# Performance work log

Measured on AMD Instinct MI355X. Metric: run time of the kernel, lower is better.

Reference implementation:

```python
import jax, jax.numpy as jnp
from jax import lax
import numpy as np

B, C, Hf, Wf = 4, 256, 64, 64
COMP = max(C // 4, 16)  # 64
SCALE, K_UP, K_ENC = 2, 5, 3
EPS = 1e-5


def setup_inputs() -> dict:
    key = jax.random.key(0)
    ks = jax.random.split(key, 6)
    x = jax.random.normal(ks[0], (B, C, Hf, Wf), dtype=jnp.float32)
    w_comp = jax.random.normal(ks[1], (COMP, C), dtype=jnp.float32) * (1.0 / np.sqrt(C))
    bn_gamma = jnp.ones((COMP,), dtype=jnp.float32)
    bn_beta = jnp.zeros((COMP,), dtype=jnp.float32)
    bn_mean = jax.random.normal(ks[2], (COMP,), dtype=jnp.float32) * 0.1
    bn_var = jax.random.uniform(ks[3], (COMP,), dtype=jnp.float32, minval=0.5, maxval=1.5)
    w_enc = jax.random.normal(ks[4], (K_UP * K_UP * SCALE * SCALE, COMP, K_ENC, K_ENC), dtype=jnp.float32) * (1.0 / np.sqrt(COMP * K_ENC * K_ENC))
    return {"x": x, "w_comp": w_comp, "bn_gamma": bn_gamma, "bn_beta": bn_beta,
            "bn_mean": bn_mean, "bn_var": bn_var, "w_enc": w_enc}


def reference(x, w_comp, bn_gamma, bn_beta, bn_mean, bn_var, w_enc):
    b, c, h, w = x.shape
    s, k = SCALE, K_UP
    # 1x1 compression conv
    comp = jnp.einsum('bchw,oc->bohw', x, w_comp)
    # BatchNorm (eval-style, running stats) + SiLU
    inv = (bn_gamma / jnp.sqrt(bn_var + EPS))[:, None, None]
    bn = (comp - bn_mean[:, None, None]) * inv + bn_beta[:, None, None]
    act = bn * jax.nn.sigmoid(bn)
    # encoder conv -> per-pixel reassembly kernels, channels = k^2 * s^2 (k2 outer, s2 inner)
    mask = lax.conv_general_dilated(act, w_enc, (1, 1), ((1, 1), (1, 1)),
                                    dimension_numbers=('NCHW', 'OIHW', 'NCHW'))
    mask = mask.reshape(b, k * k, s * s, h, w)
    mask = jax.nn.softmax(mask, axis=1)  # softmax over k_up*k_up window
    # unfold: gather 5x5 neighborhoods (pad 2), k = dy*5+dx row-major like F.unfold
    pad = k // 2
    xp = jnp.pad(x, ((0, 0), (0, 0), (pad, pad), (pad, pad)))
    patches = jnp.stack([xp[:, :, dy:dy + h, dx:dx + w]
                         for dy in range(k) for dx in range(k)], axis=2)  # (b,c,k2,h,w)
    # content-aware weighted sum per sub-pixel position
    out = jnp.einsum('bksij,bckij->bcsij', mask, patches)  # (b,c,s2,h,w)
    # s2 -> (s0,s1); pixel (i*s+s0, j*s+s1)
    out = out.reshape(b, c, s, s, h, w).transpose(0, 1, 4, 2, 5, 3).reshape(b, c, h * s, w * s)
    return out
```

## Files before the change

### kernel.cpp

```cpp
#include <hip/hip_runtime.h>
#include <hip/hip_bf16.h>
#include <hip/hip_fp16.h>
#include <math.h>

#define B_ 4
#define C_ 256
#define H_ 64
#define W_ 64
#define COMP_ 64
#define K2_ 25
#define HW_ (H_*W_)
#define EPS_ 1e-5f
#define WTE_STRIDE 26

typedef float v2f __attribute__((ext_vector_type(2)));
#define FMA2(a, b, c) __builtin_elementwise_fma((a), (b), (c))

__global__ void k_transpose(const float* __restrict__ w_comp,
                            const float* __restrict__ w_enc,
                            float* __restrict__ wTc,
                            float* __restrict__ wTe) {
    int t = blockIdx.x * 256 + threadIdx.x;
    if (t < COMP_ * C_) {
        int o = t & 63;
        int c = t >> 6;
        wTc[t] = w_comp[o * C_ + c];
    } else {
        int t2 = t - COMP_ * C_;
        if (t2 < 100 * COMP_ * 9) {
            int k2 = t2 % 25;
            int r = t2 / 25;
            int s2 = r & 3; r >>= 2;
            int q = r % 9;
            int o = r / 9;
            wTe[((o * 9 + q) * 4 + s2) * WTE_STRIDE + k2] =
                w_enc[(((k2 * 4 + s2) * COMP_) + o) * 9 + q];
        }
    }
}

__global__ void __launch_bounds__(512)
k_compress(const float* __restrict__ x, const float* __restrict__ wTc,
           const float* __restrict__ gamma, const float* __restrict__ beta,
           const float* __restrict__ mean, const float* __restrict__ var,
           float* __restrict__ act) {
    __shared__ float sx[256 * 68];
    const int tx = threadIdx.x;
    const int ty = threadIdx.y;
    const int tid = ty * 64 + tx;
    const int ogu = __builtin_amdgcn_readfirstlane(ty);
    const int b = blockIdx.y;
    const int p0 = blockIdx.x * 64;

    const float* xb = x + (size_t)b * C_ * HW_ + p0;
#pragma unroll
    for (int l = 0; l < 8; ++l) {
        int e = tid + l * 512;
        int c = e >> 4;
        int p4 = (e & 15) << 2;
        float4 v4 = *(const float4*)(xb + (size_t)c * HW_ + p4);
        *(float4*)&sx[c * 68 + p4] = v4;
    }
    __syncthreads();

    v2f acc2[4];
#pragma unroll
    for (int k = 0; k < 4; ++k) acc2[k] = (v2f){0.f, 0.f};

#pragma unroll 8
    for (int c = 0; c < 256; ++c) {
        float xv = sx[c * 68 + tx];
        const v2f* w2 = (const v2f*)(wTc + c * COMP_ + ogu * 8);
        v2f xv2 = (v2f){xv, xv};
#pragma unroll
        for (int k = 0; k < 4; ++k)
            acc2[k] = FMA2(xv2, w2[k], acc2[k]);
    }

#pragma unroll
    for (int k = 0; k < 4; ++k) {
        int o0 = ty * 8 + 2 * k;
#pragma unroll
        for (int h = 0; h < 2; ++h) {
            int o = o0 + h;
            float sv = (h == 0) ? acc2[k].x : acc2[k].y;
            float iv = gamma[o] * rsqrtf(var[o] + EPS_);
            float bn = (sv - mean[o]) * iv + beta[o];
            float sg = 1.f / (1.f + __expf(-bn));
            act[((b * COMP_ + o) * HW_) + p0 + tx] = bn * sg;
        }
    }
}

__global__ void __launch_bounds__(1024)
k_encoder(const float* __restrict__ act, const float* __restrict__ wTe,
          __half* __restrict__ maskT) {
    __shared__ float sact[13312];
    const int tx = threadIdx.x;
    const int ty = threadIdx.y;
    const int tz = threadIdx.z;
    const int tid = (tz * 4 + ty) * 64 + tx;
    const int i = blockIdx.x;
    const int b = blockIdx.y;
    const int s2u = __builtin_amdgcn_readfirstlane(ty);
    const int ogu = __builtin_amdgcn_readfirstlane(tz);

    const float* ab = act + (size_t)b * COMP_ * HW_;
    for (int t = tid; t < 3 * COMP_ * 66; t += 1024) {
        int col = t % 66;
        int r = t / 66;
        int o = r & 63;
        int row = r >> 6;
        int gi = i + row - 1;
        int gj = col - 1;
        float v = 0.f;
        if ((unsigned)gi < 64u && (unsigned)gj < 64u)
            v = ab[(o * H_ + gi) * W_ + gj];
        sact[t] = v;
    }
    __syncthreads();

    v2f acc2[13];
#pragma unroll
    for (int k = 0; k < 13; ++k) acc2[k] = (v2f){0.f, 0.f};

#pragma unroll 2
    for (int oi = 0; oi < 16; ++oi) {
        int o = ogu * 16 + oi;
#pragma unroll
        for (int q = 0; q < 9; ++q) {
            const int dy = q / 3, dx = q % 3;
            float a = sact[(dy * COMP_ + o) * 66 + tx + dx];
            const float* wb = wTe + ((o * 9 + q) * 4 + s2u) * WTE_STRIDE;
            const v2f* w2 = (const v2f*)wb;
            v2f a2 = (v2f){a, a};
#pragma unroll
            for (int k = 0; k < 12; ++k)
                acc2[k] = FMA2(a2, w2[k], acc2[k]);
            acc2[12].x = fmaf(wb[24], a, acc2[12].x);
        }
    }
    __syncthreads();

    v2f* bufA = (v2f*)sact;
    v2f* bufB = bufA + 3328;
    const int rix = ty * 64 + tx;
    if (tz == 1) {
#pragma unroll
        for (int k = 0; k < 13; ++k) bufA[k * 256 + rix] = acc2[k];
    } else if (tz == 2) {
#pragma unroll
        for (int k = 0; k < 13; ++k) bufB[k * 256 + rix] = acc2[k];
    }
    __syncthreads();
    if (tz == 0) {
#pragma unroll
        for (int k = 0; k < 13; ++k) acc2[k] += bufA[k * 256 + rix];
    } else if (tz == 3) {
#pragma unroll
        for (int k = 0; k < 13; ++k) acc2[k] += bufB[k * 256 + rix];
    }
    __syncthreads();
    if (tz == 3) {
#pragma unroll
        for (int k = 0; k < 13; ++k) bufA[k * 256 + rix] = acc2[k];
    }
    __syncthreads();
    float ex[K2_];
    if (tz == 0) {
#pragma unroll
        for (int k = 0; k < 13; ++k) acc2[k] += bufA[k * 256 + rix];

        float mx = acc2[12].x;
#pragma unroll
        for (int k = 0; k < 12; ++k) mx = fmaxf(mx, fmaxf(acc2[k].x, acc2[k].y));
        float sum = 0.f;
#pragma unroll
        for (int k = 0; k < 12; ++k) {
            ex[2 * k]     = __expf(acc2[k].x - mx);
            ex[2 * k + 1] = __expf(acc2[k].y - mx);
            sum += ex[2 * k] + ex[2 * k + 1];
        }
        ex[24] = __expf(acc2[12].x - mx);
        sum += ex[24];
        float rs = 1.f / sum;
#pragma unroll
        for (int k = 0; k < K2_; ++k) ex[k] *= rs;
    }
    __syncthreads();

    __half* st = (__half*)sact;
    if (tz == 0) {
#pragma unroll
        for (int k = 0; k < K2_; ++k)
            st[tx * 100 + k * 4 + ty] = __float2half(ex[k]);
    }
    __syncthreads();

    float4* dst = (float4*)(maskT + ((size_t)b * HW_ + i * 64) * 100);
    const float4* src = (const float4*)st;
    if (tid < 800) dst[tid] = src[tid];
}

__global__ void __launch_bounds__(256)
k_reassemble(const float* __restrict__ x, const __half* __restrict__ maskT,
             float* __restrict__ out) {
    __shared__ __align__(16) __half smask[64 * 100];
    __shared__ __align__(16) float sx[5 * 68 * 20];
    const int tx = threadIdx.x;
    const int ty = threadIdx.y;
    const int tid = ty * 64 + tx;

    const int bid = blockIdx.x;
    const int wg  = ((bid & 7) << 9) | (bid >> 3);
    const int cc = wg & 15;
    const int i  = (wg >> 4) & 63;
    const int b  = wg >> 10;

    const float4* msrc = (const float4*)(maskT + ((size_t)b * HW_ + i * 64) * 100);
    float4 vm[4];
#pragma unroll
    for (int t = 0; t < 4; ++t) {
        int e = tid + t * 256;
        vm[t] = (e < 800) ? msrc[e] : make_float4(0.f, 0.f, 0.f, 0.f);
    }

    float4 vx[6];
#pragma unroll
    for (int l = 0; l < 6; ++l) {
        int e = tid + l * 256;
        int q = e / 340;
        int rem = e - q * 340;
        int r = rem / 68;
        int col = rem - r * 68;
        int gi = i + r - 2;
        int gj = col - 2;
        float4 v = make_float4(0.f, 0.f, 0.f, 0.f);
        if (e < 1360 && (unsigned)gi < 64u && (unsigned)gj < 64u) {
            const float* p = x + ((size_t)b * C_ + cc * 16 + q * 4) * HW_ + gi * W_ + gj;
            v.x = p[0];
            v.y = p[HW_];
            v.z = p[2 * HW_];
            v.w = p[3 * HW_];
        }
        vx[l] = v;
    }

    {
        float4* mdst = (float4*)smask;
#pragma unroll
        for (int t = 0; t < 4; ++t) {
            int e = tid + t * 256;
            if (e < 800) mdst[e] = vm[t];
        }
    }
#pragma unroll
    for (int l = 0; l < 6; ++l) {
        int e = tid + l * 256;
        if (e < 1360) {
            int q = e / 340;
            int rem = e - q * 340;
            int r = rem / 68;
            int col = rem - r * 68;
            *(float4*)&sx[(r * 68 + col) * 20 + q * 4] = vx[l];
        }
    }
    __syncthreads();

    v2f a01[4], a23[4];
#pragma unroll
    for (int cl = 0; cl < 4; ++cl) { a01[cl] = (v2f){0.f, 0.f}; a23[cl] = (v2f){0.f, 0.f}; }

    float4 xq = *(const float4*)&sx[(0 * 68 + tx + 0) * 20 + ty * 4];
    __half2 h01 = *(const __half2*)&smask[tx * 100 + 0];
    __half2 h23 = *(const __half2*)&smask[tx * 100 + 2];

#pragma unroll
    for (int k2 = 0; k2 < K2_; ++k2) {
        float4 xq_c = xq;
        __half2 h01_c = h01, h23_c = h23;
        if (k2 < K2_ - 1) {
            const int kn = k2 + 1;
            const int dy = kn / 5, dx = kn % 5;
            xq  = *(const float4*)&sx[(dy * 68 + tx + dx) * 20 + ty * 4];
            h01 = *(const __half2*)&smask[tx * 100 + kn * 4];
            h23 = *(const __half2*)&smask[tx * 100 + kn * 4 + 2];
        }
        float2 f01 = __half22float2(h01_c);
        float2 f23 = __half22float2(h23_c);
        v2f m01 = (v2f){f01.x, f01.y};
        v2f m23 = (v2f){f23.x, f23.y};
        float xc[4] = {xq_c.x, xq_c.y, xq_c.z, xq_c.w};
#pragma unroll
        for (int cl = 0; cl < 4; ++cl) {
            v2f xv2 = (v2f){xc[cl], xc[cl]};
            a01[cl] = FMA2(xv2, m01, a01[cl]);
            a23[cl] = FMA2(xv2, m23, a23[cl]);
        }
    }

#pragma unroll
    for (int cl = 0; cl < 4; ++cl) {
        int c = cc * 16 + ty * 4 + cl;
        float* op = out + (((size_t)(b * C_ + c) * 128 + 2 * i) * 128) + 2 * tx;
        *(float2*)op         = float2{a01[cl].x, a01[cl].y};
        *(float2*)(op + 128) = float2{a23[cl].x, a23[cl].y};
    }
}

extern "C" void kernel_launch(void* const* d_in, const int* in_sizes, int n_in,
                              void* d_out, int out_size, void* d_ws, size_t ws_size,
                              hipStream_t stream) {
    const float* x       = (const float*)d_in[0];
    const float* w_comp  = (const float*)d_in[1];
    const float* bn_g    = (const float*)d_in[2];
    const float* bn_b    = (const float*)d_in[3];
    const float* bn_m    = (const float*)d_in[4];
    const float* bn_v    = (const float*)d_in[5];
    const float* w_enc   = (const float*)d_in[6];
    float* out = (float*)d_out;

    float* ws    = (float*)d_ws;
    float* wTc   = ws;
    float* wTe   = ws + 16384;
    float* act   = ws + 16384 + 59904;
    __half* maskT = (__half*)(act + (size_t)B_ * COMP_ * HW_);

    k_transpose<<<289, 256, 0, stream>>>(w_comp, w_enc, wTc, wTe);
    k_compress<<<dim3(64, B_), dim3(64, 8), 0, stream>>>(x, wTc, bn_g, bn_b, bn_m, bn_v, act);
    k_encoder<<<dim3(64, B_), dim3(64, 4, 4), 0, stream>>>(act, wTe, maskT);
    k_reassemble<<<4096, dim3(64, 4), 0, stream>>>(x, maskT, out);
}
```

Measured before the change: 163.4 us.

## Double-buffer reassembly with direct global-to-LDS loads and split encoder across s2 halves

The reassembly kernel becomes persistent-style. 512 blocks each loop over 8 (batch, channel-group) tiles and use double-buffered LDS filled by global_load_lds. This is meant to overlap loading the x rows and the mask with the FMA work and to cut launch and occupancy waste. The encoder grid doubles by splitting the four sub-pixel outputs across blockIdx.z, with 512-thread blocks, which raises block count but recomputes the shared activation tile load per half. The LDS layout for x changes to channel-major rows, which adds extra zero-padding passes.

```diff
diff --git a/kernel.cpp b/kernel.cpp
--- a/kernel.cpp
+++ b/kernel.cpp
@@ -15,6 +15,15 @@
 
 typedef float v2f __attribute__((ext_vector_type(2)));
 #define FMA2(a, b, c) __builtin_elementwise_fma((a), (b), (c))
+
+__device__ __forceinline__ void gload4(const void* g, void* l) {
+    __builtin_amdgcn_global_load_lds((const __attribute__((address_space(1))) void*)g,
+                                     (__attribute__((address_space(3))) void*)l, 4, 0, 0);
+}
+__device__ __forceinline__ void gload16(const void* g, void* l) {
+    __builtin_amdgcn_global_load_lds((const __attribute__((address_space(1))) void*)g,
+                                     (__attribute__((address_space(3))) void*)l, 16, 0, 0);
+}
 
 __global__ void k_transpose(const float* __restrict__ w_comp,
                             const float* __restrict__ w_enc,
@@ -92,21 +101,22 @@
     }
 }
 
-__global__ void __launch_bounds__(1024)
+__global__ void __launch_bounds__(512)
 k_encoder(const float* __restrict__ act, const float* __restrict__ wTe,
           __half* __restrict__ maskT) {
     __shared__ float sact[13312];
     const int tx = threadIdx.x;
     const int ty = threadIdx.y;
     const int tz = threadIdx.z;
-    const int tid = (tz * 4 + ty) * 64 + tx;
+    const int tid = (tz * 2 + ty) * 64 + tx;
     const int i = blockIdx.x;
     const int b = blockIdx.y;
-    const int s2u = __builtin_amdgcn_readfirstlane(ty);
+    const int s2h = blockIdx.z;
+    const int s2u = __builtin_amdgcn_readfirstlane(s2h * 2 + ty);
     const int ogu = __builtin_amdgcn_readfirstlane(tz);
 
     const float* ab = act + (size_t)b * COMP_ * HW_;
-    for (int t = tid; t < 3 * COMP_ * 66; t += 1024) {
+    for (int t = tid; t < 3 * COMP_ * 66; t += 512) {
         int col = t % 66;
         int r = t / 66;
         int o = r & 63;
@@ -143,33 +153,33 @@
     __syncthreads();
 
     v2f* bufA = (v2f*)sact;
-    v2f* bufB = bufA + 3328;
+    v2f* bufB = bufA + 13 * 128;
     const int rix = ty * 64 + tx;
     if (tz == 1) {
 #pragma unroll
-        for (int k = 0; k < 13; ++k) bufA[k * 256 + rix] = acc2[k];
+        for (int k = 0; k < 13; ++k) bufA[k * 128 + rix] = acc2[k];
     } else if (tz == 2) {
 #pragma unroll
-        for (int k = 0; k < 13; ++k) bufB[k * 256 + rix] = acc2[k];
+        for (int k = 0; k < 13; ++k) bufB[k * 128 + rix] = acc2[k];
     }
     __syncthreads();
     if (tz == 0) {
 #pragma unroll
-        for (int k = 0; k < 13; ++k) acc2[k] += bufA[k * 256 + rix];
+        for (int k = 0; k < 13; ++k) acc2[k] += bufA[k * 128 + rix];
     } else if (tz == 3) {
 #pragma unroll
-        for (int k = 0; k < 13; ++k) acc2[k] += bufB[k * 256 + rix];
+        for (int k = 0; k < 13; ++k) acc2[k] += bufB[k * 128 + rix];
     }
     __syncthreads();
     if (tz == 3) {
 #pragma unroll
-        for (int k = 0; k < 13; ++k) bufA[k * 256 + rix] = acc2[k];
+        for (int k = 0; k < 13; ++k) bufA[k * 128 + rix] = acc2[k];
     }
     __syncthreads();
     float ex[K2_];
     if (tz == 0) {
 #pragma unroll
-        for (int k = 0; k < 13; ++k) acc2[k] += bufA[k * 256 + rix];
+        for (int k = 0; k < 13; ++k) acc2[k] += bufA[k * 128 + rix];
 
         float mx = acc2[12].x;
 #pragma unroll
@@ -193,118 +203,122 @@
     if (tz == 0) {
 #pragma unroll
         for (int k = 0; k < K2_; ++k)
-            st[tx * 100 + k * 4 + ty] = __float2half(ex[k]);
-    }
-    __syncthreads();
-
-    float4* dst = (float4*)(maskT + ((size_t)b * HW_ + i * 64) * 100);
-    const float4* src = (const float4*)st;
-    if (tid < 800) dst[tid] = src[tid];
+            st[tx * 52 + k * 2 + ty] = __float2half(ex[k]);
+    }
+    __syncthreads();
+
+    __half* mrow = maskT + ((size_t)b * HW_ + i * 64) * 100 + s2h * 2;
+    for (int e = tid; e < 1600; e += 512) {
+        int j = e / 25;
+        int kk = e - j * 25;
+        *(__half2*)(mrow + j * 100 + kk * 4) = *(const __half2*)&st[j * 52 + kk * 2];
+    }
 }
 
 __global__ void __launch_bounds__(256)
 k_reassemble(const float* __restrict__ x, const __half* __restrict__ maskT,
              float* __restrict__ out) {
-    __shared__ __align__(16) __half smask[64 * 100];
-    __shared__ __align__(16) float sx[5 * 68 * 20];
+    __shared__ float sxp[2][5][16][68];
+    __shared__ __align__(16) __half smaskp[2][6400];
     const int tx = threadIdx.x;
     const int ty = threadIdx.y;
     const int tid = ty * 64 + tx;
 
     const int bid = blockIdx.x;
-    const int wg  = ((bid & 7) << 9) | (bid >> 3);
-    const int cc = wg & 15;
-    const int i  = (wg >> 4) & 63;
-    const int b  = wg >> 10;
-
-    const float4* msrc = (const float4*)(maskT + ((size_t)b * HW_ + i * 64) * 100);
-    float4 vm[4];
-#pragma unroll
-    for (int t = 0; t < 4; ++t) {
-        int e = tid + t * 256;
-        vm[t] = (e < 800) ? msrc[e] : make_float4(0.f, 0.f, 0.f, 0.f);
-    }
-
-    float4 vx[6];
-#pragma unroll
-    for (int l = 0; l < 6; ++l) {
-        int e = tid + l * 256;
-        int q = e / 340;
-        int rem = e - q * 340;
-        int r = rem / 68;
-        int col = rem - r * 68;
+    const int xcd = bid & 7;
+    const int kk  = bid >> 3;
+    const int i   = xcd * 8 + (kk & 7);
+    const int bc  = kk >> 3;
+
+    for (int e = tid; e < 640; e += 256) {
+        int d = e / 320; int rem = e - d * 320;
+        int r = rem >> 6; int rem2 = rem & 63;
+        int c = rem2 >> 2; int q = rem2 & 3;
+        int col = (q & 1) + (q >> 1) * 66;
+        sxp[d][r][c][col] = 0.f;
+    }
+#pragma unroll
+    for (int r = 0; r < 5; ++r) {
         int gi = i + r - 2;
-        int gj = col - 2;
-        float4 v = make_float4(0.f, 0.f, 0.f, 0.f);
-        if (e < 1360 && (unsigned)gi < 64u && (unsigned)gj < 64u) {
-            const float* p = x + ((size_t)b * C_ + cc * 16 + q * 4) * HW_ + gi * W_ + gj;
-            v.x = p[0];
-            v.y = p[HW_];
-            v.z = p[2 * HW_];
-            v.w = p[3 * HW_];
-        }
-        vx[l] = v;
-    }
-
-    {
-        float4* mdst = (float4*)smask;
-#pragma unroll
-        for (int t = 0; t < 4; ++t) {
-            int e = tid + t * 256;
-            if (e < 800) mdst[e] = vm[t];
-        }
-    }
-#pragma unroll
-    for (int l = 0; l < 6; ++l) {
-        int e = tid + l * 256;
-        if (e < 1360) {
-            int q = e / 340;
-            int rem = e - q * 340;
-            int r = rem / 68;
-            int col = rem - r * 68;
-            *(float4*)&sx[(r * 68 + col) * 20 + q * 4] = vx[l];
-        }
-    }
-    __syncthreads();
-
-    v2f a01[4], a23[4];
-#pragma unroll
-    for (int cl = 0; cl < 4; ++cl) { a01[cl] = (v2f){0.f, 0.f}; a23[cl] = (v2f){0.f, 0.f}; }
-
-    float4 xq = *(const float4*)&sx[(0 * 68 + tx + 0) * 20 + ty * 4];
-    __half2 h01 = *(const __half2*)&smask[tx * 100 + 0];
-    __half2 h23 = *(const __half2*)&smask[tx * 100 + 2];
-
-#pragma unroll
-    for (int k2 = 0; k2 < K2_; ++k2) {
-        float4 xq_c = xq;
-        __half2 h01_c = h01, h23_c = h23;
-        if (k2 < K2_ - 1) {
-            const int kn = k2 + 1;
-            const int dy = kn / 5, dx = kn % 5;
-            xq  = *(const float4*)&sx[(dy * 68 + tx + dx) * 20 + ty * 4];
-            h01 = *(const __half2*)&smask[tx * 100 + kn * 4];
-            h23 = *(const __half2*)&smask[tx * 100 + kn * 4 + 2];
-        }
-        float2 f01 = __half22float2(h01_c);
-        float2 f23 = __half22float2(h23_c);
-        v2f m01 = (v2f){f01.x, f01.y};
-        v2f m23 = (v2f){f23.x, f23.y};
-        float xc[4] = {xq_c.x, xq_c.y, xq_c.z, xq_c.w};
+        if ((unsigned)gi >= 64u) {
+            for (int e = tid; e < 2 * 16 * 68; e += 256) {
+                int d = e / 1088; int rem = e - d * 1088;
+                int c = rem / 68; int col = rem - c * 68;
+                sxp[d][r][c][col] = 0.f;
+            }
+        }
+    }
+
+    auto stage = [&](int n, int d) {
+        const int b  = n >> 1;
+        const int cc = bc * 2 + (n & 1);
+        const float* xit = x + ((size_t)b * C_ + cc * 16) * HW_;
+#pragma unroll
+        for (int r = 0; r < 5; ++r) {
+            int gi = i + r - 2;
+            if ((unsigned)gi < 64u) {
+#pragma unroll
+                for (int c4 = 0; c4 < 4; ++c4) {
+                    int c = (ty << 2) + c4;
+                    gload4(xit + (size_t)c * HW_ + gi * W_ + tx, &sxp[d][r][c][2]);
+                }
+            }
+        }
+        const char* mrow = (const char*)(maskT + ((size_t)b * HW_ + i * 64) * 100);
+        char* mdst = (char*)&smaskp[d][0];
+        if (ty < 3) {
+#pragma unroll
+            for (int m = 0; m < 4; ++m) {
+                int mi = ty * 4 + m;
+                gload16(mrow + mi * 1024 + tx * 16, mdst + mi * 1024);
+            }
+        } else {
+            gload4(mrow + 12288 + tx * 4, mdst + 12288);
+            gload4(mrow + 12544 + tx * 4, mdst + 12544);
+        }
+    };
+
+    stage(0, 0);
+
+#pragma unroll 1
+    for (int n = 0; n < 8; ++n) {
+        const int d = n & 1;
+        asm volatile("s_waitcnt vmcnt(0)" ::: "memory");
+        __syncthreads();
+        if (n + 1 < 8) stage(n + 1, d ^ 1);
+
+        const int b  = n >> 1;
+        const int cc = bc * 2 + (n & 1);
+
+        v2f a01[4], a23[4];
+#pragma unroll
+        for (int cl = 0; cl < 4; ++cl) { a01[cl] = (v2f){0.f, 0.f}; a23[cl] = (v2f){0.f, 0.f}; }
+
+#pragma unroll
+        for (int k2 = 0; k2 < K2_; ++k2) {
+            const int dy = k2 / 5, dx = k2 % 5;
+            __half2 h01 = *(const __half2*)&smaskp[d][tx * 100 + k2 * 4];
+            __half2 h23 = *(const __half2*)&smaskp[d][tx * 100 + k2 * 4 + 2];
+            float2 f01 = __half22float2(h01);
+            float2 f23 = __half22float2(h23);
+            v2f m01 = (v2f){f01.x, f01.y};
+            v2f m23 = (v2f){f23.x, f23.y};
+#pragma unroll
+            for (int cl = 0; cl < 4; ++cl) {
+                float xv = sxp[d][dy][(ty << 2) + cl][tx + dx];
+                v2f xv2 = (v2f){xv, xv};
+                a01[cl] = FMA2(xv2, m01, a01[cl]);
+                a23[cl] = FMA2(xv2, m23, a23[cl]);
+            }
+        }
+
 #pragma unroll
         for (int cl = 0; cl < 4; ++cl) {
-            v2f xv2 = (v2f){xc[cl], xc[cl]};
-            a01[cl] = FMA2(xv2, m01, a01[cl]);
-            a23[cl] = FMA2(xv2, m23, a23[cl]);
-        }
-    }
-
-#pragma unroll
-    for (int cl = 0; cl < 4; ++cl) {
-        int c = cc * 16 + ty * 4 + cl;
-        float* op = out + (((size_t)(b * C_ + c) * 128 + 2 * i) * 128) + 2 * tx;
-        *(float2*)op         = float2{a01[cl].x, a01[cl].y};
-        *(float2*)(op + 128) = float2{a23[cl].x, a23[cl].y};
+            int c = cc * 16 + (ty << 2) + cl;
+            float* op = out + (((size_t)(b * C_ + c) * 128 + 2 * i) * 128) + 2 * tx;
+            *(float2*)op         = float2{a01[cl].x, a01[cl].y};
+            *(float2*)(op + 128) = float2{a23[cl].x, a23[cl].y};
+        }
     }
 }
 
@@ -328,6 +342,6 @@
 
     k_transpose<<<289, 256, 0, stream>>>(w_comp, w_enc, wTc, wTe);
     k_compress<<<dim3(64, B_), dim3(64, 8), 0, stream>>>(x, wTc, bn_g, bn_b, bn_m, bn_v, act);
-    k_encoder<<<dim3(64, B_), dim3(64, 4, 4), 0, stream>>>(act, wTe, maskT);
-    k_reassemble<<<4096, dim3(64, 4), 0, stream>>>(x, maskT, out);
-}
+    k_encoder<<<dim3(64, B_, 2), dim3(64, 2, 4), 0, stream>>>(act, wTe, maskT);
+    k_reassemble<<<512, dim3(64, 4), 0, stream>>>(x, maskT, out);
+}
```

Measured after the change: 170.1 us. +4.1%, slower.
